# Kernel optimization log

Hardware: AMD Instinct MI355X
Metric: run time of the kernel (lower is better)

Reference implementation:

```python
import jax, jax.numpy as jnp
import numpy as np

B, T, D = 4, 2048, 1024

def setup_inputs() -> dict:
    key = jax.random.key(0)
    kx, kq, kk, kv = jax.random.split(key, 4)
    lim = 1.0 / np.sqrt(D)
    x = jax.random.normal(kx, (B, T, D), dtype=jnp.float32)
    # nn.Linear weights (stored as [out,in]); applied as x @ W.T
    W_q = jax.random.uniform(kq, (D, D), jnp.float32, -lim, lim)
    W_k = jax.random.uniform(kk, (D, D), jnp.float32, -lim, lim)
    W_v = jax.random.uniform(kv, (D, D), jnp.float32, -lim, lim)
    return {"x": x, "W_q": W_q, "W_k": W_k, "W_v": W_v}

def reference(x, W_q, W_k, W_v):
    d = x.shape[-1]
    Q = jnp.einsum('btd,ed->bte', x, W_q)
    K = jnp.einsum('btd,ed->bte', x, W_k)
    V = jnp.einsum('btd,ed->bte', x, W_v)
    att = jnp.einsum('bqd,bkd->bqk', Q, K) / jnp.sqrt(jnp.asarray(d, x.dtype))
    weights = jax.nn.softmax(att, axis=-1)  # NOTE: original applies no causal mask
    return jnp.einsum('bqk,bkd->bqd', weights, V)
```

## Files before the change

kernel.cpp:

```cpp
#include <hip/hip_runtime.h>
#include <hip/hip_bf16.h>
#include <math.h>
#include <type_traits>


typedef short shortx8 __attribute__((ext_vector_type(8)));
typedef short shortx4 __attribute__((ext_vector_type(4)));
typedef float floatx16 __attribute__((ext_vector_type(16)));
typedef __attribute__((address_space(3))) void lds_void_t;
typedef __attribute__((address_space(1))) const void gmem_void_t;

#define GLD16(gp, lp) \
    __builtin_amdgcn_global_load_lds((gmem_void_t*)(gp), (lds_void_t*)(lp), 16, 0, 0)

#define MODE_PROJ 0
#define MODE_EXP  1
#define MODE_DIV  2

template <int MODE>
__global__ __launch_bounds__(256) void mfma_gemm_abt(
    const __hip_bfloat16* __restrict__ A, const __hip_bfloat16* __restrict__ B,
    void* __restrict__ Cv, float* __restrict__ rowsum,
    __hip_bfloat16* __restrict__ Vt,
    int M, int N, int K, long sA, long sB, long sC, float alpha)
{
    __shared__ __hip_bfloat16 As[128 * 32];
    __shared__ __hip_bfloat16 Bs[128 * 32];

    using CT = std::conditional_t<MODE == MODE_DIV, float, __hip_bfloat16>;

    const int z = blockIdx.z;
    A += (long)z * sA;
    B += (long)z * sB;
    CT* C = (CT*)Cv + (long)z * sC;

    const int t     = threadIdx.x;
    const int wave  = t >> 6;
    const int lane  = t & 63;
    const int m0    = blockIdx.x * 128;
    const int n0    = blockIdx.y * 128;
    const int wm    = (wave >> 1) * 64;
    const int wn    = (wave & 1) * 64;
    const int lrow  = lane & 31;
    const int lhalf = lane >> 5;

    const int srow = t >> 2;
    const int fs   = ((t >> 2) & 3) ^ ((t >> 4) & 1);
    const int scol = (((t & 3) ^ fs)) * 8;

    const int fr = (lrow & 3) ^ ((lrow >> 2) & 1);

    floatx16 acc[2][2] = {};

    for (int k0 = 0; k0 < K; k0 += 32) {
        GLD16(A + (long)(m0 + srow) * K + k0 + scol,      As + wave * 512);
        GLD16(A + (long)(m0 + 64 + srow) * K + k0 + scol, As + 2048 + wave * 512);
        GLD16(B + (long)(n0 + srow) * K + k0 + scol,      Bs + wave * 512);
        GLD16(B + (long)(n0 + 64 + srow) * K + k0 + scol, Bs + 2048 + wave * 512);
        __syncthreads();

        #pragma unroll
        for (int h = 0; h < 2; ++h) {
            const int koff = (((2 * h + lhalf) ^ fr)) * 8;
            shortx8 af[2], bf[2];
            #pragma unroll
            for (int i = 0; i < 2; ++i)
                af[i] = *(const shortx8*)(As + (wm + 32 * i + lrow) * 32 + koff);
            #pragma unroll
            for (int j = 0; j < 2; ++j)
                bf[j] = *(const shortx8*)(Bs + (wn + 32 * j + lrow) * 32 + koff);
            #pragma unroll
            for (int i = 0; i < 2; ++i)
                #pragma unroll
                for (int j = 0; j < 2; ++j)
                    acc[i][j] = __builtin_amdgcn_mfma_f32_32x32x16_bf16(
                        af[i], bf[j], acc[i][j], 0, 0, 0);
        }
        __syncthreads();
    }

    if constexpr (MODE == MODE_PROJ) {
        if (z == 2) {
            const int bz   = m0 >> 11;
            const long bo  = (long)bz * N * 2048;
            #pragma unroll
            for (int i = 0; i < 2; ++i)
                #pragma unroll
                for (int j = 0; j < 2; ++j)
                    #pragma unroll
                    for (int g = 0; g < 4; ++g) {
                        const int trow = (m0 + wm + 32 * i + g * 8 + 4 * lhalf) & 2047;
                        const long col = n0 + wn + 32 * j + lrow;
                        shortx4 pk;
                        #pragma unroll
                        for (int r = 0; r < 4; ++r) {
                            __hip_bfloat16 hb = __float2bfloat16(acc[i][j][4 * g + r]);
                            pk[r] = *(short*)&hb;
                        }
                        *(shortx4*)(Vt + bo + col * 2048 + trow) = pk;
                    }
        } else {
            #pragma unroll
            for (int i = 0; i < 2; ++i)
                #pragma unroll
                for (int j = 0; j < 2; ++j)
                    #pragma unroll
                    for (int g = 0; g < 4; ++g)
                        #pragma unroll
                        for (int r = 0; r < 4; ++r) {
                            const long row = m0 + wm + 32 * i + g * 8 + 4 * lhalf + r;
                            const long col = n0 + wn + 32 * j + lrow;
                            C[row * N + col] = __float2bfloat16(acc[i][j][4 * g + r]);
                        }
        }
    } else if constexpr (MODE == MODE_EXP) {
        #pragma unroll
        for (int i = 0; i < 2; ++i) {
            float rs[16];
            #pragma unroll
            for (int reg = 0; reg < 16; ++reg) rs[reg] = 0.0f;
            #pragma unroll
            for (int j = 0; j < 2; ++j)
                #pragma unroll
                for (int g = 0; g < 4; ++g)
                    #pragma unroll
                    for (int r = 0; r < 4; ++r) {
                        const long row = m0 + wm + 32 * i + g * 8 + 4 * lhalf + r;
                        const long col = n0 + wn + 32 * j + lrow;
                        const float e = __expf(acc[i][j][4 * g + r] * alpha);
                        rs[4 * g + r] += e;
                        C[row * N + col] = __float2bfloat16(e);
                    }
            #pragma unroll
            for (int reg = 0; reg < 16; ++reg) {
                float v = rs[reg];
                v += __shfl_xor(v, 1);
                v += __shfl_xor(v, 2);
                v += __shfl_xor(v, 4);
                v += __shfl_xor(v, 8);
                v += __shfl_xor(v, 16);
                if (lrow == 0) {
                    const long row = m0 + wm + 32 * i + (reg >> 2) * 8 + 4 * lhalf + (reg & 3);
                    atomicAdd(&rowsum[(long)z * M + row], v);
                }
            }
        }
    } else {
        #pragma unroll
        for (int i = 0; i < 2; ++i) {
            float inv[16];
            #pragma unroll
            for (int g = 0; g < 4; ++g)
                #pragma unroll
                for (int r = 0; r < 4; ++r) {
                    const long row = m0 + wm + 32 * i + g * 8 + 4 * lhalf + r;
                    inv[4 * g + r] = 1.0f / rowsum[(long)z * M + row];
                }
            #pragma unroll
            for (int j = 0; j < 2; ++j)
                #pragma unroll
                for (int g = 0; g < 4; ++g)
                    #pragma unroll
                    for (int r = 0; r < 4; ++r) {
                        const long row = m0 + wm + 32 * i + g * 8 + 4 * lhalf + r;
                        const long col = n0 + wn + 32 * j + lrow;
                        C[row * N + col] = acc[i][j][4 * g + r] * inv[4 * g + r];
                    }
        }
    }
}

__global__ __launch_bounds__(256) void prep(
    const float* __restrict__ x,
    const float* __restrict__ W0, const float* __restrict__ W1,
    const float* __restrict__ W2,
    __hip_bfloat16* __restrict__ xb, __hip_bfloat16* __restrict__ Wb,
    float* __restrict__ rowsum, int n4x, int n4w)
{
    const long i = (long)blockIdx.x * 256 + threadIdx.x;
    if (i < 2048) {
        float4 zz; zz.x = zz.y = zz.z = zz.w = 0.0f;
        ((float4*)rowsum)[i] = zz;
    }
    const float* src;
    __hip_bfloat16* dst;
    long j;
    if (i < n4x) {
        src = x; dst = xb; j = i;
    } else {
        const long k = i - n4x;
        const int w  = (int)(k >> 18);
        j = k & (n4w - 1);
        src = (w == 0) ? W0 : (w == 1) ? W1 : W2;
        dst = Wb + (long)w * n4w * 4;
    }
    const float4 f = ((const float4*)src)[j];
    dst[j * 4 + 0] = __float2bfloat16(f.x);
    dst[j * 4 + 1] = __float2bfloat16(f.y);
    dst[j * 4 + 2] = __float2bfloat16(f.z);
    dst[j * 4 + 3] = __float2bfloat16(f.w);
}

extern "C" void kernel_launch(void* const* d_in, const int* in_sizes, int n_in,
                              void* d_out, int out_size, void* d_ws, size_t ws_size,
                              hipStream_t stream)
{
    constexpr int  Bb = 4, T = 2048, D = 1024;
    constexpr int  M  = Bb * T;
    constexpr long TD = (long)T * D;
    constexpr long TT = (long)T * T;
    constexpr long MD = (long)M * D;

    const float* x  = (const float*)d_in[0];
    const float* Wq = (const float*)d_in[1];
    const float* Wk = (const float*)d_in[2];
    const float* Wv = (const float*)d_in[3];
    float* out = (float*)d_out;

    __hip_bfloat16* Q  = (__hip_bfloat16*)d_ws;
    __hip_bfloat16* Kb = Q + MD;
    __hip_bfloat16* Vt = Kb + MD;
    __hip_bfloat16* P  = Vt + MD;
    __hip_bfloat16* xb = P + (long)Bb * TT;
    __hip_bfloat16* Wb = xb + MD;
    float*     rowsum  = (float*)(Wb + 3L * D * D);

    dim3 blk(256);

    constexpr int n4x = (int)(MD / 4);
    constexpr int n4w = D * D / 4;
    prep<<<dim3((n4x + 3 * n4w) / 256), blk, 0, stream>>>(
        x, Wq, Wk, Wv, xb, Wb, rowsum, n4x, n4w);

    mfma_gemm_abt<MODE_PROJ><<<dim3(M / 128, D / 128, 3), blk, 0, stream>>>(
        xb, Wb, Q, nullptr, Vt, M, D, D, 0, (long)D * D, MD, 1.0f);

    mfma_gemm_abt<MODE_EXP><<<dim3(T / 128, T / 128, Bb), blk, 0, stream>>>(
        Q, Kb, P, rowsum, nullptr, T, T, D, TD, TD, TT, 0.03125f);

    mfma_gemm_abt<MODE_DIV><<<dim3(T / 128, D / 128, Bb), blk, 0, stream>>>(
        P, Vt, out, rowsum, nullptr, T, D, T, TT, TD, TD, 1.0f);

    (void)in_sizes; (void)n_in; (void)out_size; (void)ws_size;
}
```

Measured before the change: 278.8 us.

## Double-buffer LDS tiles to overlap global loads with MFMA compute

Replaces the single A/B shared-memory tiles with two ping-pong buffers, so the next K-slice is issued via global_load_lds while the current slice is consumed by MFMAs. This cuts one barrier per iteration and is meant to hide global-memory latency behind compute. It doubles LDS use to 32 KB per block, which may reduce occupancy. Correctness relies on the single barrier also covering completion of the asynchronous LDS loads.

```diff
diff --git a/kernel.cpp b/kernel.cpp
--- a/kernel.cpp
+++ b/kernel.cpp
@@ -24,8 +24,7 @@
     __hip_bfloat16* __restrict__ Vt,
     int M, int N, int K, long sA, long sB, long sC, float alpha)
 {
-    __shared__ __hip_bfloat16 As[128 * 32];
-    __shared__ __hip_bfloat16 Bs[128 * 32];
+    __shared__ __hip_bfloat16 SB[4 * 4096];
 
     using CT = std::conditional_t<MODE == MODE_DIV, float, __hip_bfloat16>;
 
@@ -46,29 +45,32 @@
 
     const int srow = t >> 2;
     const int fs   = ((t >> 2) & 3) ^ ((t >> 4) & 1);
-    const int scol = (((t & 3) ^ fs)) * 8;
-
-    const int fr = (lrow & 3) ^ ((lrow >> 2) & 1);
+    const int scol = ((t & 3) ^ fs) * 8;
+    const int fr   = (lrow & 3) ^ ((lrow >> 2) & 1);
 
     floatx16 acc[2][2] = {};
 
-    for (int k0 = 0; k0 < K; k0 += 32) {
-        GLD16(A + (long)(m0 + srow) * K + k0 + scol,      As + wave * 512);
-        GLD16(A + (long)(m0 + 64 + srow) * K + k0 + scol, As + 2048 + wave * 512);
-        GLD16(B + (long)(n0 + srow) * K + k0 + scol,      Bs + wave * 512);
-        GLD16(B + (long)(n0 + 64 + srow) * K + k0 + scol, Bs + 2048 + wave * 512);
-        __syncthreads();
-
+    auto stage = [&](int k0, int p) {
+        __hip_bfloat16* Asb = SB + p * 4096;
+        __hip_bfloat16* Bsb = SB + 8192 + p * 4096;
+        GLD16(A + (long)(m0 + srow) * K + k0 + scol,      Asb + wave * 512);
+        GLD16(A + (long)(m0 + 64 + srow) * K + k0 + scol, Asb + 2048 + wave * 512);
+        GLD16(B + (long)(n0 + srow) * K + k0 + scol,      Bsb + wave * 512);
+        GLD16(B + (long)(n0 + 64 + srow) * K + k0 + scol, Bsb + 2048 + wave * 512);
+    };
+    auto compute = [&](int p) {
+        const __hip_bfloat16* Asb = SB + p * 4096;
+        const __hip_bfloat16* Bsb = SB + 8192 + p * 4096;
         #pragma unroll
         for (int h = 0; h < 2; ++h) {
-            const int koff = (((2 * h + lhalf) ^ fr)) * 8;
+            const int koff = ((2 * h + lhalf) ^ fr) * 8;
             shortx8 af[2], bf[2];
             #pragma unroll
             for (int i = 0; i < 2; ++i)
-                af[i] = *(const shortx8*)(As + (wm + 32 * i + lrow) * 32 + koff);
+                af[i] = *(const shortx8*)(Asb + (wm + 32 * i + lrow) * 32 + koff);
             #pragma unroll
             for (int j = 0; j < 2; ++j)
-                bf[j] = *(const shortx8*)(Bs + (wn + 32 * j + lrow) * 32 + koff);
+                bf[j] = *(const shortx8*)(Bsb + (wn + 32 * j + lrow) * 32 + koff);
             #pragma unroll
             for (int i = 0; i < 2; ++i)
                 #pragma unroll
@@ -76,8 +78,18 @@
                     acc[i][j] = __builtin_amdgcn_mfma_f32_32x32x16_bf16(
                         af[i], bf[j], acc[i][j], 0, 0, 0);
         }
+    };
+
+    stage(0, 0);
+    __syncthreads();
+    int p = 0;
+    for (int k0 = 32; k0 < K; k0 += 32) {
+        stage(k0, p ^ 1);
+        compute(p);
         __syncthreads();
-    }
+        p ^= 1;
+    }
+    compute(p);
 
     if constexpr (MODE == MODE_PROJ) {
         if (z == 2) {
```

Result: faster. 269.7 us (-3.3%).
